# Kernel optimization log

Hardware: AMD Instinct MI355X
Metric: run time of the kernel (lower is better)

Reference implementation:

```python
import jax, jax.numpy as jnp
import numpy as np

B, C, H, W = 4, 512, 64, 64
C8 = C // 8


def setup_inputs() -> dict:
    key = jax.random.key(0)
    ks = jax.random.split(key, 8)
    s = 0.02
    return {
        "x": jax.random.normal(ks[0], (B, C, H, W), dtype=jnp.float32),
        "wq": jax.random.normal(ks[1], (C8, C), dtype=jnp.float32) * s,
        "bq": jax.random.normal(ks[2], (C8,), dtype=jnp.float32) * s,
        "wk": jax.random.normal(ks[3], (C8, C), dtype=jnp.float32) * s,
        "bk": jax.random.normal(ks[4], (C8,), dtype=jnp.float32) * s,
        "wv": jax.random.normal(ks[5], (C, C), dtype=jnp.float32) * s,
        "bv": jax.random.normal(ks[6], (C,), dtype=jnp.float32) * s,
        "gamma": jax.random.normal(ks[7], (1,), dtype=jnp.float32),
    }


def reference(x, wq, bq, wk, bk, wv, bv, gamma):
    b, c, h, w = x.shape
    # 1x1 convs == per-pixel linear projections
    q = jnp.einsum('bchw,oc->bohw', x, wq) + bq[None, :, None, None]  # [B,C8,H,W]
    k = jnp.einsum('bchw,oc->bohw', x, wk) + bk[None, :, None, None]  # [B,C8,H,W]
    v = jnp.einsum('bchw,oc->bohw', x, wv) + bv[None, :, None, None]  # [B,C,H,W]
    qf = q.reshape(b, c // 8, h * w)  # [B,C8,HW]
    kf = k.reshape(b, c // 8, h * w)  # [B,C8,HW]
    # energy[b,i,j] = q_i . k_j, viewed as [B,H,W,H,W]; softmax over last dim
    energy = jnp.einsum('bci,bcj->bij', qf, kf).reshape(b, h, w, h, w)
    attn = jax.nn.softmax(energy, axis=-1)  # [B,H,W,H2,W2]
    # torch: out = bmm(value, permute(0,1,3,2,4).view(B,HW,HW))
    # rows index (h,h2) into value's spatial grid; cols index output (w,w2)
    out = jnp.einsum('bchk,bhwkv->bcwv', v, attn)  # [B,C,H,W]
    return gamma * out + x
```

## Files before the change

kernel.cpp:

```cpp
#include <hip/hip_runtime.h>
#include <hip/hip_bf16.h>


typedef __bf16 bf16_t;
typedef __bf16 bf16x8 __attribute__((ext_vector_type(8)));
typedef __bf16 bf16x4 __attribute__((ext_vector_type(4)));
typedef float f32x4 __attribute__((ext_vector_type(4)));

#define HW_ 4096
#define CIN 512
#define CQ 64

__device__ __forceinline__ void gload16(const void* g, void* l) {
  __builtin_amdgcn_global_load_lds((const __attribute__((address_space(1))) void*)g,
                                   (__attribute__((address_space(3))) void*)l, 16, 0, 0);
}

__global__ __launch_bounds__(256) void k_wcat(const float* __restrict__ wq,
                                              const float* __restrict__ wk,
                                              const float* __restrict__ wv,
                                              bf16_t* __restrict__ Wcat) {
  int idx = (blockIdx.x * 256 + threadIdx.x) * 4;
  int row = idx >> 9, c = idx & 511;
  const float* src;
  if (row < 64)       src = wq + row * 512 + c;
  else if (row < 128) src = wk + (row - 64) * 512 + c;
  else                src = wv + (row - 128) * 512 + c;
  float4 v = *(const float4*)src;
  bf16x4 o = { (bf16_t)v.x, (bf16_t)v.y, (bf16_t)v.z, (bf16_t)v.w };
  *(bf16x4*)&Wcat[idx] = o;
}

__global__ __launch_bounds__(256) void k_prep(const float* __restrict__ x, bf16_t* __restrict__ xT) {
  __shared__ float tile[64][65];
  const int b = blockIdx.z;
  const int p0 = blockIdx.x * 64, c0 = blockIdx.y * 64;
  const float* xb = x + (size_t)b * CIN * HW_;
  bf16_t* xTb = xT + (size_t)b * HW_ * CIN;
  const int tid = threadIdx.x;
  const int r = tid >> 4, q = tid & 15;
#pragma unroll
  for (int i = 0; i < 4; ++i) {
    int lr = r + 16 * i;
    float4 v = *(const float4*)&xb[(size_t)(c0 + lr) * HW_ + p0 + q * 4];
    tile[lr][q * 4 + 0] = v.x; tile[lr][q * 4 + 1] = v.y;
    tile[lr][q * 4 + 2] = v.z; tile[lr][q * 4 + 3] = v.w;
  }
  __syncthreads();
#pragma unroll
  for (int i = 0; i < 4; ++i) {
    int pr = r + 16 * i;
    bf16x4 o;
    o[0] = (bf16_t)tile[q * 4 + 0][pr];
    o[1] = (bf16_t)tile[q * 4 + 1][pr];
    o[2] = (bf16_t)tile[q * 4 + 2][pr];
    o[3] = (bf16_t)tile[q * 4 + 3][pr];
    *(bf16x4*)&xTb[(size_t)(p0 + pr) * CIN + c0 + q * 4] = o;
  }
}

__global__ __launch_bounds__(256) void k_projqk(const bf16_t* __restrict__ Wcat,
                                                const bf16_t* __restrict__ xT,
                                                const float* __restrict__ bq,
                                                const float* __restrict__ bk,
                                                bf16_t* __restrict__ qfT,
                                                bf16_t* __restrict__ kfT) {
  __shared__ bf16_t As[128][64];
  __shared__ bf16_t Bs[128][64];
  const int b = blockIdx.z;
  const int n0 = blockIdx.x * 128;
  const char* Wb = (const char*)Wcat;
  const char* Xb = (const char*)(xT + (size_t)b * HW_ * CIN);
  const int tid = threadIdx.x, wv_ = tid >> 6, lane = tid & 63;
  const int wm = wv_ >> 1, wn = wv_ & 1;
  const int g = lane >> 4, cc = lane & 15;
  f32x4 acc[4][4]{};
  for (int ks = 0; ks < 512; ks += 64) {
    if (ks) __syncthreads();
#pragma unroll
    for (int i = 0; i < 4; ++i) {
      int ch = wv_ * 4 + i;
      int rr = ch * 8 + (lane >> 3);
      int sl = (lane & 7) ^ (rr & 7);
      gload16(Wb + (size_t)rr * 1024 + ks * 2 + sl * 16, (char*)As + ch * 1024);
      gload16(Xb + (size_t)(n0 + rr) * 1024 + ks * 2 + sl * 16, (char*)Bs + ch * 1024);
    }
    __syncthreads();
#pragma unroll
    for (int k2 = 0; k2 < 2; ++k2) {
      bf16x8 a[4], bb[4];
#pragma unroll
      for (int f = 0; f < 4; ++f)
        a[f] = *(const bf16x8*)((char*)As + (wm * 64 + f * 16 + cc) * 128 + (((k2 * 4 + g) ^ (cc & 7)) * 16));
#pragma unroll
      for (int f = 0; f < 4; ++f)
        bb[f] = *(const bf16x8*)((char*)Bs + (wn * 64 + f * 16 + cc) * 128 + (((k2 * 4 + g) ^ (cc & 7)) * 16));
#pragma unroll
      for (int fm = 0; fm < 4; ++fm)
#pragma unroll
        for (int fn = 0; fn < 4; ++fn)
          acc[fm][fn] = __builtin_amdgcn_mfma_f32_16x16x32_bf16(a[fm], bb[fn], acc[fm][fn], 0, 0, 0);
    }
  }
  bf16_t* qb = qfT + (size_t)b * HW_ * CQ;
  bf16_t* kb = kfT + (size_t)b * HW_ * CQ;
#pragma unroll
  for (int fm = 0; fm < 4; ++fm) {
#pragma unroll
    for (int j = 0; j < 4; ++j) {
      int m = wm * 64 + fm * 16 + g * 4 + j;
      float bias = (m < 64) ? bq[m] : bk[m - 64];
#pragma unroll
      for (int fn = 0; fn < 4; ++fn) {
        int n = n0 + wn * 64 + fn * 16 + cc;
        float val = acc[fm][fn][j] + bias;
        if (m < 64) qb[(size_t)n * CQ + m] = (bf16_t)val;
        else        kb[(size_t)n * CQ + (m - 64)] = (bf16_t)val;
      }
    }
  }
}

__global__ __launch_bounds__(256) void k_projv(const bf16_t* __restrict__ Wcat,
                                               const bf16_t* __restrict__ xT,
                                               const float* __restrict__ bv,
                                               bf16_t* __restrict__ Vp2) {
  __shared__ bf16_t As[128][64];
  __shared__ bf16_t Bs[128][64];
  const int b = blockIdx.z;
  const int n0 = blockIdx.x * 128, m0 = blockIdx.y * 128;
  const char* Wb = (const char*)Wcat;
  const char* Xb = (const char*)(xT + (size_t)b * HW_ * CIN);
  const int tid = threadIdx.x, wv_ = tid >> 6, lane = tid & 63;
  const int wm = wv_ >> 1, wn = wv_ & 1;
  const int g = lane >> 4, cc = lane & 15;
  f32x4 acc[4][4]{};
  for (int ks = 0; ks < 512; ks += 64) {
    if (ks) __syncthreads();
#pragma unroll
    for (int i = 0; i < 4; ++i) {
      int ch = wv_ * 4 + i;
      int rr = ch * 8 + (lane >> 3);
      int sl = (lane & 7) ^ (rr & 7);
      int pix = (rr & 63) * 64 + (blockIdx.x * 2) + (rr >> 6);
      gload16(Wb + (size_t)(128 + m0 + rr) * 1024 + ks * 2 + sl * 16, (char*)As + ch * 1024);
      gload16(Xb + (size_t)pix * 1024 + ks * 2 + sl * 16, (char*)Bs + ch * 1024);
    }
    __syncthreads();
#pragma unroll
    for (int k2 = 0; k2 < 2; ++k2) {
      bf16x8 a[4], bb[4];
#pragma unroll
      for (int f = 0; f < 4; ++f)
        a[f] = *(const bf16x8*)((char*)As + (wm * 64 + f * 16 + cc) * 128 + (((k2 * 4 + g) ^ (cc & 7)) * 16));
#pragma unroll
      for (int f = 0; f < 4; ++f)
        bb[f] = *(const bf16x8*)((char*)Bs + (wn * 64 + f * 16 + cc) * 128 + (((k2 * 4 + g) ^ (cc & 7)) * 16));
#pragma unroll
      for (int fm = 0; fm < 4; ++fm)
#pragma unroll
        for (int fn = 0; fn < 4; ++fn)
          acc[fm][fn] = __builtin_amdgcn_mfma_f32_16x16x32_bf16(a[fm], bb[fn], acc[fm][fn], 0, 0, 0);
    }
  }
  bf16_t* Vb = Vp2 + (size_t)b * CIN * HW_;
#pragma unroll
  for (int fm = 0; fm < 4; ++fm) {
#pragma unroll
    for (int j = 0; j < 4; ++j) {
      int m = m0 + wm * 64 + fm * 16 + g * 4 + j;
      float bias = bv[m];
#pragma unroll
      for (int fn = 0; fn < 4; ++fn) {
        int n = n0 + wn * 64 + fn * 16 + cc;
        Vb[(size_t)m * HW_ + n] = (bf16_t)(acc[fm][fn][j] + bias);
      }
    }
  }
}

__global__ __launch_bounds__(256) void k_energy(const bf16_t* __restrict__ qfT,
                                                const bf16_t* __restrict__ kfT,
                                                bf16_t* __restrict__ Pt, int zbase) {
  __shared__ bf16_t As[128][64];
  __shared__ bf16_t Bs[64][64];
  const int b = zbase + blockIdx.z;
  const int w0 = blockIdx.x * 2, ky = blockIdx.y;
  const char* qb = (const char*)(qfT + (size_t)b * HW_ * CQ);
  const char* kb = (const char*)(kfT + (size_t)b * HW_ * CQ);
  bf16_t* Ptb = Pt + (size_t)blockIdx.z * 16777216;
  const int tid = threadIdx.x, wv_ = tid >> 6, lane = tid & 63;
  const int g = lane >> 4, cc = lane & 15;
  f32x4 acc[2][4]{};
#pragma unroll
  for (int i = 0; i < 4; ++i) {
    int ch = wv_ * 4 + i;
    int rr = ch * 8 + (lane >> 3);
    int sl = (lane & 7) ^ (rr & 7);
    int pix = (rr & 63) * 64 + w0 + (rr >> 6);
    gload16(qb + (size_t)pix * 128 + sl * 16, (char*)As + ch * 1024);
  }
#pragma unroll
  for (int i = 0; i < 2; ++i) {
    int ch = wv_ * 2 + i;
    int rr = ch * 8 + (lane >> 3);
    int sl = (lane & 7) ^ (rr & 7);
    gload16(kb + (size_t)(ky * 64 + rr) * 128 + sl * 16, (char*)Bs + ch * 1024);
  }
  __syncthreads();
#pragma unroll
  for (int k2 = 0; k2 < 2; ++k2) {
    bf16x8 a[2], bb[4];
#pragma unroll
    for (int f = 0; f < 2; ++f)
      a[f] = *(const bf16x8*)((char*)As + (wv_ * 32 + f * 16 + cc) * 128 + (((k2 * 4 + g) ^ (cc & 7)) * 16));
#pragma unroll
    for (int f = 0; f < 4; ++f)
      bb[f] = *(const bf16x8*)((char*)Bs + (f * 16 + cc) * 128 + (((k2 * 4 + g) ^ (cc & 7)) * 16));
#pragma unroll
    for (int fm = 0; fm < 2; ++fm)
#pragma unroll
      for (int fn = 0; fn < 4; ++fn)
        acc[fm][fn] = __builtin_amdgcn_mfma_f32_16x16x32_bf16(a[fm], bb[fn], acc[fm][fn], 0, 0, 0);
  }
  const int w = w0 + (wv_ >> 1);
#pragma unroll
  for (int fm = 0; fm < 2; ++fm) {
    float e[4][4], invj[4];
#pragma unroll
    for (int j = 0; j < 4; ++j) {
      float mx = fmaxf(fmaxf(acc[fm][0][j], acc[fm][1][j]), fmaxf(acc[fm][2][j], acc[fm][3][j]));
#pragma unroll
      for (int d = 1; d < 16; d <<= 1) mx = fmaxf(mx, __shfl_xor(mx, d, 64));
      float s = 0.f;
#pragma unroll
      for (int fn = 0; fn < 4; ++fn) { e[fn][j] = __expf(acc[fm][fn][j] - mx); s += e[fn][j]; }
#pragma unroll
      for (int d = 1; d < 16; d <<= 1) s += __shfl_xor(s, d, 64);
      invj[j] = __builtin_amdgcn_rcpf(s);
    }
    int h0 = (wv_ & 1) * 32 + fm * 16 + g * 4;
#pragma unroll
    for (int fn = 0; fn < 4; ++fn) {
      int v = fn * 16 + cc;
      bf16x4 pk = { (bf16_t)(e[fn][0] * invj[0]), (bf16_t)(e[fn][1] * invj[1]),
                    (bf16_t)(e[fn][2] * invj[2]), (bf16_t)(e[fn][3] * invj[3]) };
      *(bf16x4*)&Ptb[(((size_t)w * 64 + ky) * 64 + v) * 64 + h0] = pk;
    }
  }
}

__global__ __launch_bounds__(256) void k_out(const bf16_t* __restrict__ Vp2,
                                             const bf16_t* __restrict__ Pt,
                                             const float* __restrict__ x,
                                             const float* __restrict__ gamma,
                                             float* __restrict__ outp, int zbase) {
  __shared__ char Ls[65536];
  const int lin = blockIdx.x + (blockIdx.y << 2) + (blockIdx.z << 7);
  const int nwg8 = (gridDim.z == 4) ? 64 : 16;
  const int rsw = (lin & 7) * nwg8 + (lin >> 3);
  const int c0 = (rsw & 3) * 128;
  const int w0 = ((rsw >> 2) & 31) * 2;
  const int bz = (gridDim.z == 4) ? (rsw >> 7) : 0;
  const int b = zbase + bz;
  const char* Vb = (const char*)(Vp2 + (size_t)b * CIN * HW_);
  const char* Pb = (const char*)(Pt + (size_t)bz * 16777216);
  const int tid = threadIdx.x, wv_ = tid >> 6, lane = tid & 63;
  const int wm = wv_ >> 1, wn = wv_ & 1;
  const int g = lane >> 4, cc = lane & 15;

  const char* aSb[4]; const char* bSb[4];
#pragma unroll
  for (int r = 0; r < 4; ++r) {
    int L = (r * 4 + wv_) * 64 + lane;
    int arow = L >> 3, asl = (L & 7) ^ (arow & 7);
    aSb[r] = Vb + (size_t)(c0 + arow) * 8192 + asl * 16;
    int ws = L >> 9, e = L & 511, v = e >> 3, bsl = (e & 7) ^ (v & 7);
    bSb[r] = Pb + (size_t)(w0 + ws) * 524288 + v * 128 + bsl * 16;
  }
  int aoff[2][4], boff[2][4];
#pragma unroll
  for (int k2 = 0; k2 < 2; ++k2) {
#pragma unroll
    for (int fm = 0; fm < 4; ++fm)
      aoff[k2][fm] = (wm * 64 + fm * 16 + cc) * 128 + (((k2 * 4 + g) ^ (cc & 7)) * 16);
#pragma unroll
    for (int fn = 0; fn < 4; ++fn)
      boff[k2][fn] = 16384 + wn * 8192 + (fn * 16 + cc) * 128 + (((k2 * 4 + g) ^ (cc & 7)) * 16);
  }

  f32x4 acc[4][4]{};
  {
    char* base = Ls;
#pragma unroll
    for (int r = 0; r < 4; ++r) gload16(aSb[r], base + (r * 4 + wv_) * 1024);
#pragma unroll
    for (int r = 0; r < 4; ++r) gload16(bSb[r], base + 16384 + (r * 4 + wv_) * 1024);
  }
  for (int s = 0; s < 64; ++s) {
    if (s < 63) {
      char* base = Ls + ((s + 1) & 1) * 32768;
#pragma unroll
      for (int r = 0; r < 4; ++r) gload16(aSb[r] + (size_t)(s + 1) * 128, base + (r * 4 + wv_) * 1024);
#pragma unroll
      for (int r = 0; r < 4; ++r) gload16(bSb[r] + (size_t)(s + 1) * 8192, base + 16384 + (r * 4 + wv_) * 1024);
      asm volatile("s_waitcnt vmcnt(8)" ::: "memory");
    } else {
      asm volatile("s_waitcnt vmcnt(0)" ::: "memory");
    }
    __builtin_amdgcn_s_barrier();
    const char* base = Ls + (s & 1) * 32768;
#pragma unroll
    for (int k2 = 0; k2 < 2; ++k2) {
      bf16x8 a[4], bb[4];
#pragma unroll
      for (int fm = 0; fm < 4; ++fm) a[fm] = *(const bf16x8*)(base + aoff[k2][fm]);
#pragma unroll
      for (int fn = 0; fn < 4; ++fn) bb[fn] = *(const bf16x8*)(base + boff[k2][fn]);
#pragma unroll
      for (int fm = 0; fm < 4; ++fm)
#pragma unroll
        for (int fn = 0; fn < 4; ++fn)
          acc[fm][fn] = __builtin_amdgcn_mfma_f32_16x16x32_bf16(a[fm], bb[fn], acc[fm][fn], 0, 0, 0);
    }
    asm volatile("s_waitcnt lgkmcnt(0)" ::: "memory");
    __builtin_amdgcn_s_barrier();
  }
  const float gmm = gamma[0];
  const float* xb = x + (size_t)b * CIN * HW_;
  float* ob = outp + (size_t)b * CIN * HW_;
  const int w = w0 + wn;
#pragma unroll
  for (int fm = 0; fm < 4; ++fm) {
#pragma unroll
    for (int jj = 0; jj < 4; ++jj) {
      int c = c0 + wm * 64 + fm * 16 + g * 4 + jj;
#pragma unroll
      for (int fn = 0; fn < 4; ++fn) {
        int n = w * 64 + fn * 16 + cc;
        size_t idx = (size_t)c * HW_ + n;
        ob[idx] = gmm * acc[fm][fn][jj] + xb[idx];
      }
    }
  }
}

extern "C" void kernel_launch(void* const* d_in, const int* in_sizes, int n_in,
                              void* d_out, int out_size, void* d_ws, size_t ws_size,
                              hipStream_t stream) {
  const float* x  = (const float*)d_in[0];
  const float* wq = (const float*)d_in[1];
  const float* bq = (const float*)d_in[2];
  const float* wk = (const float*)d_in[3];
  const float* bk = (const float*)d_in[4];
  const float* wv = (const float*)d_in[5];
  const float* bv = (const float*)d_in[6];
  const float* gamma = (const float*)d_in[7];
  float* outp = (float*)d_out;
  char* ws = (char*)d_ws;
  size_t off = 0;
  bf16_t* xT   = (bf16_t*)(ws + off); off += (size_t)4 * HW_ * CIN * 2;
  bf16_t* Wcat = (bf16_t*)(ws + off); off += (size_t)640 * CIN * 2;
  bf16_t* qfT  = (bf16_t*)(ws + off); off += (size_t)4 * HW_ * CQ * 2;
  bf16_t* kfT  = (bf16_t*)(ws + off); off += (size_t)4 * HW_ * CQ * 2;
  bf16_t* Vp2  = (bf16_t*)(ws + off); off += (size_t)4 * CIN * HW_ * 2;
  bf16_t* Pt   = (bf16_t*)(ws + off);
  const size_t pbytes = (size_t)HW_ * HW_ * 2;
  const bool full = (ws_size >= off + 4 * pbytes);

  k_wcat<<<dim3(320), dim3(256), 0, stream>>>(wq, wk, wv, Wcat);
  k_prep<<<dim3(64, 8, 4), dim3(256), 0, stream>>>(x, xT);
  k_projqk<<<dim3(32, 1, 4), dim3(256), 0, stream>>>(Wcat, xT, bq, bk, qfT, kfT);
  k_projv<<<dim3(32, 4, 4), dim3(256), 0, stream>>>(Wcat, xT, bv, Vp2);
  if (full) {
    k_energy<<<dim3(32, 64, 4), dim3(256), 0, stream>>>(qfT, kfT, Pt, 0);
    k_out<<<dim3(4, 32, 4), dim3(256), 0, stream>>>(Vp2, Pt, x, gamma, outp, 0);
  } else {
    for (int b = 0; b < 4; ++b) {
      k_energy<<<dim3(32, 64, 1), dim3(256), 0, stream>>>(qfT, kfT, Pt, b);
      k_out<<<dim3(4, 32, 1), dim3(256), 0, stream>>>(Vp2, Pt, x, gamma, outp, b);
    }
  }
}
```

Before: 179.3 us.

## Fuse energy softmax into output GEMM, recomputing attention tiles in LDS

Merges the energy/softmax kernel into the output GEMM. Each block now recomputes its QK^T tile for each K-step, applies softmax in registers, and writes the probabilities to LDS instead of materializing the 128 MB attention matrix in global memory. The softmax also drops the max subtraction, which is numerically risky if energies are large. The cost is redundant energy recomputation: each of the 4 channel-tile blocks recomputes the same attention, and each step gains an extra barrier. LDS use rises to 80 KB per block.

```diff
diff --git a/kernel.cpp b/kernel.cpp
--- a/kernel.cpp
+++ b/kernel.cpp
@@ -179,144 +179,146 @@
   }
 }
 
-__global__ __launch_bounds__(256) void k_energy(const bf16_t* __restrict__ qfT,
-                                                const bf16_t* __restrict__ kfT,
-                                                bf16_t* __restrict__ Pt, int zbase) {
-  __shared__ bf16_t As[128][64];
-  __shared__ bf16_t Bs[64][64];
-  const int b = zbase + blockIdx.z;
-  const int w0 = blockIdx.x * 2, ky = blockIdx.y;
+__global__ __launch_bounds__(256) void k_att(const bf16_t* __restrict__ qfT,
+                                             const bf16_t* __restrict__ kfT,
+                                             const bf16_t* __restrict__ Vp2,
+                                             const float* __restrict__ x,
+                                             const float* __restrict__ gamma,
+                                             float* __restrict__ outp) {
+  __shared__ char Ls[81920];
+  const int lin = blockIdx.x + (blockIdx.y << 2) + (blockIdx.z << 7);
+  const int rsw = (lin & 7) * 64 + (lin >> 3);
+  const int c0 = (rsw & 3) * 128;
+  const int w0 = ((rsw >> 2) & 31) * 2;
+  const int b = rsw >> 7;
   const char* qb = (const char*)(qfT + (size_t)b * HW_ * CQ);
   const char* kb = (const char*)(kfT + (size_t)b * HW_ * CQ);
-  bf16_t* Ptb = Pt + (size_t)blockIdx.z * 16777216;
+  const char* Vb = (const char*)(Vp2 + (size_t)b * CIN * HW_);
   const int tid = threadIdx.x, wv_ = tid >> 6, lane = tid & 63;
+  const int wm = wv_ >> 1, wn = wv_ & 1;
   const int g = lane >> 4, cc = lane & 15;
-  f32x4 acc[2][4]{};
+  const int ws = wv_ >> 1;
+
+  const char* aSb[4];
+  const char* kSb[2];
+#pragma unroll
+  for (int r = 0; r < 4; ++r) {
+    int L = (r * 4 + wv_) * 64 + lane;
+    int arow = L >> 3, asl = (L & 7) ^ (arow & 7);
+    aSb[r] = Vb + (size_t)(c0 + arow) * 8192 + asl * 16;
+  }
+#pragma unroll
+  for (int i = 0; i < 2; ++i) {
+    int ch = wv_ * 2 + i;
+    int rr = ch * 8 + (lane >> 3);
+    int sl = (lane & 7) ^ (rr & 7);
+    kSb[i] = kb + (size_t)rr * 128 + sl * 16;
+  }
+
+  int aoff[2][4], koff[2][4], boff[2][4];
+#pragma unroll
+  for (int k2 = 0; k2 < 2; ++k2) {
+#pragma unroll
+    for (int fm = 0; fm < 4; ++fm)
+      aoff[k2][fm] = (wm * 64 + fm * 16 + cc) * 128 + (((k2 * 4 + g) ^ (cc & 7)) * 16);
+#pragma unroll
+    for (int fn = 0; fn < 4; ++fn) {
+      koff[k2][fn] = 32768 + (fn * 16 + cc) * 128 + (((k2 * 4 + g) ^ (cc & 7)) * 16);
+      boff[k2][fn] = 65536 + wn * 8192 + (fn * 16 + cc) * 128 + (((k2 * 4 + g) ^ (cc & 7)) * 16);
+    }
+  }
+  int poff[2][4];
+#pragma unroll
+  for (int fm = 0; fm < 2; ++fm) {
+    int h0 = (wv_ & 1) * 32 + fm * 16 + g * 4;
+#pragma unroll
+    for (int fn = 0; fn < 4; ++fn) {
+      int v = fn * 16 + cc;
+      poff[fm][fn] = 65536 + ws * 8192 + v * 128 + (((h0 >> 3) ^ (v & 7)) * 16) + (h0 & 7) * 2;
+    }
+  }
+
 #pragma unroll
   for (int i = 0; i < 4; ++i) {
     int ch = wv_ * 4 + i;
     int rr = ch * 8 + (lane >> 3);
     int sl = (lane & 7) ^ (rr & 7);
     int pix = (rr & 63) * 64 + w0 + (rr >> 6);
-    gload16(qb + (size_t)pix * 128 + sl * 16, (char*)As + ch * 1024);
-  }
-#pragma unroll
-  for (int i = 0; i < 2; ++i) {
-    int ch = wv_ * 2 + i;
-    int rr = ch * 8 + (lane >> 3);
-    int sl = (lane & 7) ^ (rr & 7);
-    gload16(kb + (size_t)(ky * 64 + rr) * 128 + sl * 16, (char*)Bs + ch * 1024);
-  }
-  __syncthreads();
-#pragma unroll
-  for (int k2 = 0; k2 < 2; ++k2) {
-    bf16x8 a[2], bb[4];
-#pragma unroll
-    for (int f = 0; f < 2; ++f)
-      a[f] = *(const bf16x8*)((char*)As + (wv_ * 32 + f * 16 + cc) * 128 + (((k2 * 4 + g) ^ (cc & 7)) * 16));
-#pragma unroll
-    for (int f = 0; f < 4; ++f)
-      bb[f] = *(const bf16x8*)((char*)Bs + (f * 16 + cc) * 128 + (((k2 * 4 + g) ^ (cc & 7)) * 16));
-#pragma unroll
-    for (int fm = 0; fm < 2; ++fm)
-#pragma unroll
-      for (int fn = 0; fn < 4; ++fn)
-        acc[fm][fn] = __builtin_amdgcn_mfma_f32_16x16x32_bf16(a[fm], bb[fn], acc[fm][fn], 0, 0, 0);
-  }
-  const int w = w0 + (wv_ >> 1);
-#pragma unroll
-  for (int fm = 0; fm < 2; ++fm) {
-    float e[4][4], invj[4];
-#pragma unroll
-    for (int j = 0; j < 4; ++j) {
-      float mx = fmaxf(fmaxf(acc[fm][0][j], acc[fm][1][j]), fmaxf(acc[fm][2][j], acc[fm][3][j]));
-#pragma unroll
-      for (int d = 1; d < 16; d <<= 1) mx = fmaxf(mx, __shfl_xor(mx, d, 64));
-      float s = 0.f;
-#pragma unroll
-      for (int fn = 0; fn < 4; ++fn) { e[fn][j] = __expf(acc[fm][fn][j] - mx); s += e[fn][j]; }
-#pragma unroll
-      for (int d = 1; d < 16; d <<= 1) s += __shfl_xor(s, d, 64);
-      invj[j] = __builtin_amdgcn_rcpf(s);
-    }
-    int h0 = (wv_ & 1) * 32 + fm * 16 + g * 4;
-#pragma unroll
-    for (int fn = 0; fn < 4; ++fn) {
-      int v = fn * 16 + cc;
-      bf16x4 pk = { (bf16_t)(e[fn][0] * invj[0]), (bf16_t)(e[fn][1] * invj[1]),
-                    (bf16_t)(e[fn][2] * invj[2]), (bf16_t)(e[fn][3] * invj[3]) };
-      *(bf16x4*)&Ptb[(((size_t)w * 64 + ky) * 64 + v) * 64 + h0] = pk;
-    }
-  }
-}
-
-__global__ __launch_bounds__(256) void k_out(const bf16_t* __restrict__ Vp2,
-                                             const bf16_t* __restrict__ Pt,
-                                             const float* __restrict__ x,
-                                             const float* __restrict__ gamma,
-                                             float* __restrict__ outp, int zbase) {
-  __shared__ char Ls[65536];
-  const int lin = blockIdx.x + (blockIdx.y << 2) + (blockIdx.z << 7);
-  const int nwg8 = (gridDim.z == 4) ? 64 : 16;
-  const int rsw = (lin & 7) * nwg8 + (lin >> 3);
-  const int c0 = (rsw & 3) * 128;
-  const int w0 = ((rsw >> 2) & 31) * 2;
-  const int bz = (gridDim.z == 4) ? (rsw >> 7) : 0;
-  const int b = zbase + bz;
-  const char* Vb = (const char*)(Vp2 + (size_t)b * CIN * HW_);
-  const char* Pb = (const char*)(Pt + (size_t)bz * 16777216);
-  const int tid = threadIdx.x, wv_ = tid >> 6, lane = tid & 63;
-  const int wm = wv_ >> 1, wn = wv_ & 1;
-  const int g = lane >> 4, cc = lane & 15;
-
-  const char* aSb[4]; const char* bSb[4];
-#pragma unroll
-  for (int r = 0; r < 4; ++r) {
-    int L = (r * 4 + wv_) * 64 + lane;
-    int arow = L >> 3, asl = (L & 7) ^ (arow & 7);
-    aSb[r] = Vb + (size_t)(c0 + arow) * 8192 + asl * 16;
-    int ws = L >> 9, e = L & 511, v = e >> 3, bsl = (e & 7) ^ (v & 7);
-    bSb[r] = Pb + (size_t)(w0 + ws) * 524288 + v * 128 + bsl * 16;
-  }
-  int aoff[2][4], boff[2][4];
-#pragma unroll
-  for (int k2 = 0; k2 < 2; ++k2) {
-#pragma unroll
-    for (int fm = 0; fm < 4; ++fm)
-      aoff[k2][fm] = (wm * 64 + fm * 16 + cc) * 128 + (((k2 * 4 + g) ^ (cc & 7)) * 16);
-#pragma unroll
-    for (int fn = 0; fn < 4; ++fn)
-      boff[k2][fn] = 16384 + wn * 8192 + (fn * 16 + cc) * 128 + (((k2 * 4 + g) ^ (cc & 7)) * 16);
-  }
+    gload16(qb + (size_t)pix * 128 + sl * 16, Ls + 49152 + ch * 1024);
+  }
+#pragma unroll
+  for (int r = 0; r < 4; ++r) gload16(aSb[r], Ls + (r * 4 + wv_) * 1024);
+#pragma unroll
+  for (int i = 0; i < 2; ++i) gload16(kSb[i], Ls + 32768 + (wv_ * 2 + i) * 1024);
+  asm volatile("s_waitcnt vmcnt(0)" ::: "memory");
+  __builtin_amdgcn_s_barrier();
+
+  bf16x8 qf[2][2];
+#pragma unroll
+  for (int fm = 0; fm < 2; ++fm)
+#pragma unroll
+    for (int k2 = 0; k2 < 2; ++k2)
+      qf[fm][k2] = *(const bf16x8*)(Ls + 49152 + (wv_ * 32 + fm * 16 + cc) * 128 +
+                                    (((k2 * 4 + g) ^ (cc & 7)) * 16));
 
   f32x4 acc[4][4]{};
-  {
-    char* base = Ls;
-#pragma unroll
-    for (int r = 0; r < 4; ++r) gload16(aSb[r], base + (r * 4 + wv_) * 1024);
-#pragma unroll
-    for (int r = 0; r < 4; ++r) gload16(bSb[r], base + 16384 + (r * 4 + wv_) * 1024);
-  }
   for (int s = 0; s < 64; ++s) {
+    const int cur = s & 1, nxt = cur ^ 1;
     if (s < 63) {
-      char* base = Ls + ((s + 1) & 1) * 32768;
-#pragma unroll
-      for (int r = 0; r < 4; ++r) gload16(aSb[r] + (size_t)(s + 1) * 128, base + (r * 4 + wv_) * 1024);
-#pragma unroll
-      for (int r = 0; r < 4; ++r) gload16(bSb[r] + (size_t)(s + 1) * 8192, base + 16384 + (r * 4 + wv_) * 1024);
-      asm volatile("s_waitcnt vmcnt(8)" ::: "memory");
+#pragma unroll
+      for (int r = 0; r < 4; ++r)
+        gload16(aSb[r] + (size_t)(s + 1) * 128, Ls + nxt * 16384 + (r * 4 + wv_) * 1024);
+#pragma unroll
+      for (int i = 0; i < 2; ++i)
+        gload16(kSb[i] + (size_t)(s + 1) * 8192, Ls + 32768 + nxt * 8192 + (wv_ * 2 + i) * 1024);
+      asm volatile("s_waitcnt vmcnt(6)" ::: "memory");
     } else {
       asm volatile("s_waitcnt vmcnt(0)" ::: "memory");
     }
     __builtin_amdgcn_s_barrier();
-    const char* base = Ls + (s & 1) * 32768;
+
+    f32x4 eacc[2][4]{};
+#pragma unroll
+    for (int k2 = 0; k2 < 2; ++k2) {
+      bf16x8 kf[4];
+#pragma unroll
+      for (int fn = 0; fn < 4; ++fn)
+        kf[fn] = *(const bf16x8*)(Ls + cur * 8192 + koff[k2][fn]);
+#pragma unroll
+      for (int fm = 0; fm < 2; ++fm)
+#pragma unroll
+        for (int fn = 0; fn < 4; ++fn)
+          eacc[fm][fn] = __builtin_amdgcn_mfma_f32_16x16x32_bf16(qf[fm][k2], kf[fn], eacc[fm][fn], 0, 0, 0);
+    }
+#pragma unroll
+    for (int fm = 0; fm < 2; ++fm) {
+      float e[4][4], invj[4];
+#pragma unroll
+      for (int j = 0; j < 4; ++j) {
+        float sum = 0.f;
+#pragma unroll
+        for (int fn = 0; fn < 4; ++fn) { e[fn][j] = __expf(eacc[fm][fn][j]); sum += e[fn][j]; }
+#pragma unroll
+        for (int d = 1; d < 16; d <<= 1) sum += __shfl_xor(sum, d, 64);
+        invj[j] = __builtin_amdgcn_rcpf(sum);
+      }
+#pragma unroll
+      for (int fn = 0; fn < 4; ++fn) {
+        bf16x4 pk = { (bf16_t)(e[fn][0] * invj[0]), (bf16_t)(e[fn][1] * invj[1]),
+                      (bf16_t)(e[fn][2] * invj[2]), (bf16_t)(e[fn][3] * invj[3]) };
+        *(bf16x4*)(Ls + poff[fm][fn]) = pk;
+      }
+    }
+    asm volatile("s_waitcnt lgkmcnt(0)" ::: "memory");
+    __builtin_amdgcn_s_barrier();
+
 #pragma unroll
     for (int k2 = 0; k2 < 2; ++k2) {
       bf16x8 a[4], bb[4];
 #pragma unroll
-      for (int fm = 0; fm < 4; ++fm) a[fm] = *(const bf16x8*)(base + aoff[k2][fm]);
-#pragma unroll
-      for (int fn = 0; fn < 4; ++fn) bb[fn] = *(const bf16x8*)(base + boff[k2][fn]);
+      for (int fm = 0; fm < 4; ++fm) a[fm] = *(const bf16x8*)(Ls + cur * 16384 + aoff[k2][fm]);
+#pragma unroll
+      for (int fn = 0; fn < 4; ++fn) bb[fn] = *(const bf16x8*)(Ls + boff[k2][fn]);
 #pragma unroll
       for (int fm = 0; fm < 4; ++fm)
 #pragma unroll
@@ -326,6 +328,7 @@
     asm volatile("s_waitcnt lgkmcnt(0)" ::: "memory");
     __builtin_amdgcn_s_barrier();
   }
+
   const float gmm = gamma[0];
   const float* xb = x + (size_t)b * CIN * HW_;
   float* ob = outp + (size_t)b * CIN * HW_;
@@ -363,22 +366,11 @@
   bf16_t* Wcat = (bf16_t*)(ws + off); off += (size_t)640 * CIN * 2;
   bf16_t* qfT  = (bf16_t*)(ws + off); off += (size_t)4 * HW_ * CQ * 2;
   bf16_t* kfT  = (bf16_t*)(ws + off); off += (size_t)4 * HW_ * CQ * 2;
-  bf16_t* Vp2  = (bf16_t*)(ws + off); off += (size_t)4 * CIN * HW_ * 2;
-  bf16_t* Pt   = (bf16_t*)(ws + off);
-  const size_t pbytes = (size_t)HW_ * HW_ * 2;
-  const bool full = (ws_size >= off + 4 * pbytes);
+  bf16_t* Vp2  = (bf16_t*)(ws + off);
 
   k_wcat<<<dim3(320), dim3(256), 0, stream>>>(wq, wk, wv, Wcat);
   k_prep<<<dim3(64, 8, 4), dim3(256), 0, stream>>>(x, xT);
   k_projqk<<<dim3(32, 1, 4), dim3(256), 0, stream>>>(Wcat, xT, bq, bk, qfT, kfT);
   k_projv<<<dim3(32, 4, 4), dim3(256), 0, stream>>>(Wcat, xT, bv, Vp2);
-  if (full) {
-    k_energy<<<dim3(32, 64, 4), dim3(256), 0, stream>>>(qfT, kfT, Pt, 0);
-    k_out<<<dim3(4, 32, 4), dim3(256), 0, stream>>>(Vp2, Pt, x, gamma, outp, 0);
-  } else {
-    for (int b = 0; b < 4; ++b) {
-      k_energy<<<dim3(32, 64, 1), dim3(256), 0, stream>>>(qfT, kfT, Pt, b);
-      k_out<<<dim3(4, 32, 1), dim3(256), 0, stream>>>(Vp2, Pt, x, gamma, outp, b);
-    }
-  }
-}
+  k_att<<<dim3(4, 32, 4), dim3(256), 0, stream>>>(qfT, kfT, Vp2, x, gamma, outp);
+}
```

Measured after the change: 224.5 us. 25.2% more time.
